# Performance work log

Measured on AMD Instinct MI355X. Metric: run time of the kernel, lower is better.

The kernel has to match this reference:

```python
import jax, jax.numpy as jnp
import numpy as np

B, L, D = 2, 8192, 1024


def setup_inputs() -> dict:
    key = jax.random.key(0)
    ks = jax.random.split(key, 6)
    x = jax.random.normal(ks[0], (B, L, D), dtype=jnp.float32)
    # phazor param init (torch): exp(2j*pi*arange(D)/D) * |randn(D)|
    mag = jnp.abs(jax.random.normal(ks[1], (D,), dtype=jnp.float32))
    ang = (2.0 * np.pi * jnp.arange(D) / D).astype(jnp.float32)
    phazor_real = mag * jnp.cos(ang)
    phazor_imag = mag * jnp.sin(ang)
    # phazor_init ~ complex randn
    phazor_init_real = jax.random.normal(ks[2], (D,), dtype=jnp.float32)
    phazor_init_imag = jax.random.normal(ks[3], (D,), dtype=jnp.float32)
    # last_conv_init ~ complex randn (first-call hidden state, broadcast over batch)
    last_conv_real = jax.random.normal(ks[4], (D,), dtype=jnp.float32)
    last_conv_imag = jax.random.normal(ks[5], (D,), dtype=jnp.float32)
    return {
        "x": x,
        "phazor_real": phazor_real, "phazor_imag": phazor_imag,
        "phazor_init_real": phazor_init_real, "phazor_init_imag": phazor_init_imag,
        "last_conv_real": last_conv_real, "last_conv_imag": last_conv_imag,
    }


def reference(x, phazor_real, phazor_imag, phazor_init_real, phazor_init_imag,
              last_conv_real, last_conv_imag):
    b, length, dim = x.shape
    dtype = x.dtype
    # reparameterized decay: magnitude exp(-|p|^2), keep angle of p
    ph = jnp.exp(-(phazor_real * phazor_real + phazor_imag * phazor_imag)) \
         * jnp.exp(1j * jnp.arctan2(phazor_imag, phazor_real))          # [D] complex
    # phazor_progression[t, d] = ph[d] ** t
    prog = jnp.power(ph[None, :], jnp.arange(length)[:, None])           # [L, D]
    pinit = phazor_init_real + 1j * phazor_init_imag                     # [D]
    filt = prog * pinit[None, :]                                         # [L, D]
    # FFT convolution with zero-padding to 2L (linear convolution)
    filt_fft = jnp.fft.fft(filt, n=2 * length, axis=0)                   # [2L, D]
    x_fft = jnp.fft.fft(x.astype(jnp.complex64), n=2 * length, axis=1)   # [B, 2L, D]
    conv = jnp.fft.ifft(filt_fft[None, :, :] * x_fft, axis=1)[:, :length, :]  # [B, L, D]
    # carry in hidden state from previous chunk (here: learned init, broadcast over batch)
    last = (last_conv_real + 1j * last_conv_imag)[None, None, :]          # [1, 1, D]
    conv_with_past = conv + last * prog[None, :, :] * ph[None, None, :]
    return conv_with_past.real.astype(dtype)
```

## Files before the change

### kernel.cpp

```cpp
#include <hip/hip_runtime.h>

#define BB 2
#define LL 8192
#define DD 1024
#define NC 128
#define TT 64

__device__ __forceinline__ void compute_ph(float pr, float pi, float& phr, float& phi) {
    float r2 = fmaf(pr, pr, pi * pi);
    float mag = expf(-r2);
    float r = sqrtf(r2);
    if (r > 1e-30f) {
        float inv = mag / r;
        phr = pr * inv;
        phi = pi * inv;
    } else {
        phr = mag;
        phi = 0.0f;
    }
}

__global__ __launch_bounds__(256) void k_partial(
    const float* __restrict__ x,
    const float* __restrict__ pr, const float* __restrict__ pi,
    const float* __restrict__ qr, const float* __restrict__ qi,
    float2* __restrict__ partial)
{
    int d = blockIdx.x * 256 + threadIdx.x;
    int j = blockIdx.y;
    int b = blockIdx.z;
    float phr, phi; compute_ph(pr[d], pi[d], phr, phi);
    float qre = qr[d], qim = qi[d];
    const float* xp = x + ((size_t)b * LL + (size_t)j * TT) * DD + d;
    float sr = 0.f, si = 0.f;
    #pragma unroll 16
    for (int t = 0; t < TT; ++t) {
        float xv = xp[(size_t)t * DD];
        float nr = fmaf(phr, sr, fmaf(-phi, si, qre * xv));
        float ni = fmaf(phi, sr, fmaf(phr, si, qim * xv));
        sr = nr; si = ni;
    }
    partial[((size_t)b * NC + j) * DD + d] = make_float2(sr, si);
}

__global__ __launch_bounds__(256) void k_final(
    const float* __restrict__ x,
    const float* __restrict__ pr, const float* __restrict__ pi,
    const float* __restrict__ qr, const float* __restrict__ qi,
    const float* __restrict__ lr, const float* __restrict__ li,
    const float2* __restrict__ partial,
    float* __restrict__ out)
{
    int d = blockIdx.x * 256 + threadIdx.x;
    int j = blockIdx.y;
    int b = blockIdx.z;
    float phr, phi; compute_ph(pr[d], pi[d], phr, phi);
    float qre = qr[d], qim = qi[d];

    float ar = phr, ai = phi;
    #pragma unroll
    for (int k = 0; k < 6; ++k) {
        float nr = ar * ar - ai * ai;
        float ni = 2.f * ar * ai;
        ar = nr; ai = ni;
    }

    float Sr = lr[d], Si = li[d];
    const float2* pb = partial + (size_t)b * NC * DD + d;
    #pragma unroll 4
    for (int k = 0; k < j; ++k) {
        float2 P = pb[(size_t)k * DD];
        float nr = fmaf(ar, Sr, fmaf(-ai, Si, P.x));
        float ni = fmaf(ai, Sr, fmaf(ar, Si, P.y));
        Sr = nr; Si = ni;
    }

    const size_t base = ((size_t)b * LL + (size_t)j * TT) * DD + d;
    const float* xp = x + base;
    float* op = out + base;
    #pragma unroll 16
    for (int t = 0; t < TT; ++t) {
        float xv = xp[(size_t)t * DD];
        float nr = fmaf(phr, Sr, fmaf(-phi, Si, qre * xv));
        float ni = fmaf(phi, Sr, fmaf(phr, Si, qim * xv));
        Sr = nr; Si = ni;
        op[(size_t)t * DD] = nr;
    }
}

extern "C" void kernel_launch(void* const* d_in, const int* in_sizes, int n_in,
                              void* d_out, int out_size, void* d_ws, size_t ws_size,
                              hipStream_t stream) {
    const float* x  = (const float*)d_in[0];
    const float* pr = (const float*)d_in[1];
    const float* pi = (const float*)d_in[2];
    const float* qr = (const float*)d_in[3];
    const float* qi = (const float*)d_in[4];
    const float* lr = (const float*)d_in[5];
    const float* li = (const float*)d_in[6];
    float* out = (float*)d_out;

    float2* partial = (float2*)d_ws;

    dim3 grid(DD / 256, NC, BB);
    k_partial<<<grid, 256, 0, stream>>>(x, pr, pi, qr, qi, partial);
    k_final<<<grid, 256, 0, stream>>>(x, pr, pi, qr, qi, lr, li, partial, out);
}
```

Baseline: 46.07 us.

## Split chunk-prefix carry into dedicated sequential scan kernel with prefetching

After: 51.68 us. 1.12x slower.

```diff
diff --git a/kernel.cpp b/kernel.cpp
--- a/kernel.cpp
+++ b/kernel.cpp
@@ -43,20 +43,18 @@
     partial[((size_t)b * NC + j) * DD + d] = make_float2(sr, si);
 }
 
-__global__ __launch_bounds__(256) void k_final(
-    const float* __restrict__ x,
+#define SCAN_DEPTH 16
+__global__ __launch_bounds__(256) void k_scan(
     const float* __restrict__ pr, const float* __restrict__ pi,
-    const float* __restrict__ qr, const float* __restrict__ qi,
     const float* __restrict__ lr, const float* __restrict__ li,
     const float2* __restrict__ partial,
-    float* __restrict__ out)
+    float2* __restrict__ Sarr)
 {
-    int d = blockIdx.x * 256 + threadIdx.x;
-    int j = blockIdx.y;
-    int b = blockIdx.z;
+    int idx = blockIdx.x * 256 + threadIdx.x;
+    int d = idx & (DD - 1);
+    int b = idx >> 10;
+
     float phr, phi; compute_ph(pr[d], pi[d], phr, phi);
-    float qre = qr[d], qim = qi[d];
-
     float ar = phr, ai = phi;
     #pragma unroll
     for (int k = 0; k < 6; ++k) {
@@ -67,13 +65,50 @@
 
     float Sr = lr[d], Si = li[d];
     const float2* pb = partial + (size_t)b * NC * DD + d;
-    #pragma unroll 4
-    for (int k = 0; k < j; ++k) {
-        float2 P = pb[(size_t)k * DD];
-        float nr = fmaf(ar, Sr, fmaf(-ai, Si, P.x));
-        float ni = fmaf(ai, Sr, fmaf(ar, Si, P.y));
-        Sr = nr; Si = ni;
+    float2* sb = Sarr + (size_t)b * NC * DD + d;
+
+    float2 buf[SCAN_DEPTH];
+    #pragma unroll
+    for (int u = 0; u < SCAN_DEPTH; ++u) buf[u] = pb[(size_t)u * DD];
+
+    #pragma unroll
+    for (int r = 0; r < NC / SCAN_DEPTH; ++r) {
+        float2 nxt[SCAN_DEPTH];
+        if (r < NC / SCAN_DEPTH - 1) {
+            #pragma unroll
+            for (int u = 0; u < SCAN_DEPTH; ++u)
+                nxt[u] = pb[(size_t)((r + 1) * SCAN_DEPTH + u) * DD];
+        }
+        #pragma unroll
+        for (int u = 0; u < SCAN_DEPTH; ++u) {
+            int j = r * SCAN_DEPTH + u;
+            sb[(size_t)j * DD] = make_float2(Sr, Si);
+            float nr = fmaf(ar, Sr, fmaf(-ai, Si, buf[u].x));
+            float ni = fmaf(ai, Sr, fmaf(ar, Si, buf[u].y));
+            Sr = nr; Si = ni;
+        }
+        if (r < NC / SCAN_DEPTH - 1) {
+            #pragma unroll
+            for (int u = 0; u < SCAN_DEPTH; ++u) buf[u] = nxt[u];
+        }
     }
+}
+
+__global__ __launch_bounds__(256) void k_final(
+    const float* __restrict__ x,
+    const float* __restrict__ pr, const float* __restrict__ pi,
+    const float* __restrict__ qr, const float* __restrict__ qi,
+    const float2* __restrict__ Sarr,
+    float* __restrict__ out)
+{
+    int d = blockIdx.x * 256 + threadIdx.x;
+    int j = blockIdx.y;
+    int b = blockIdx.z;
+    float phr, phi; compute_ph(pr[d], pi[d], phr, phi);
+    float qre = qr[d], qim = qi[d];
+
+    float2 S = Sarr[((size_t)b * NC + j) * DD + d];
+    float Sr = S.x, Si = S.y;
 
     const size_t base = ((size_t)b * LL + (size_t)j * TT) * DD + d;
     const float* xp = x + base;
@@ -84,7 +119,7 @@
         float nr = fmaf(phr, Sr, fmaf(-phi, Si, qre * xv));
         float ni = fmaf(phi, Sr, fmaf(phr, Si, qim * xv));
         Sr = nr; Si = ni;
-        op[(size_t)t * DD] = nr;
+        __builtin_nontemporal_store(nr, &op[(size_t)t * DD]);
     }
 }
 
@@ -101,8 +136,10 @@
     float* out = (float*)d_out;
 
     float2* partial = (float2*)d_ws;
+    float2* Sarr    = partial + (size_t)BB * NC * DD;
 
     dim3 grid(DD / 256, NC, BB);
     k_partial<<<grid, 256, 0, stream>>>(x, pr, pi, qr, qi, partial);
-    k_final<<<grid, 256, 0, stream>>>(x, pr, pi, qr, qi, lr, li, partial, out);
+    k_scan<<<(BB * DD) / 256, 256, 0, stream>>>(pr, pi, lr, li, partial, Sarr);
+    k_final<<<grid, 256, 0, stream>>>(x, pr, pi, qr, qi, Sarr, out);
 }
```

## Fuse partial and final scan kernels with a grid barrier, caching x in registers

Applied to the files above, without the earlier changes.

New measurement: 107.0 us. 2.32x slower.

```diff
diff --git a/kernel.cpp b/kernel.cpp
--- a/kernel.cpp
+++ b/kernel.cpp
@@ -3,8 +3,9 @@
 #define BB 2
 #define LL 8192
 #define DD 1024
-#define NC 128
-#define TT 64
+#define NC 64
+#define TT 128
+#define NBLK ((DD / 256) * NC * BB)
 
 __device__ __forceinline__ void compute_ph(float pr, float pi, float& phr, float& phi) {
     float r2 = fmaf(pr, pr, pi * pi);
@@ -20,46 +21,54 @@
     }
 }
 
-__global__ __launch_bounds__(256) void k_partial(
-    const float* __restrict__ x,
-    const float* __restrict__ pr, const float* __restrict__ pi,
-    const float* __restrict__ qr, const float* __restrict__ qi,
-    float2* __restrict__ partial)
-{
-    int d = blockIdx.x * 256 + threadIdx.x;
-    int j = blockIdx.y;
-    int b = blockIdx.z;
-    float phr, phi; compute_ph(pr[d], pi[d], phr, phi);
-    float qre = qr[d], qim = qi[d];
-    const float* xp = x + ((size_t)b * LL + (size_t)j * TT) * DD + d;
-    float sr = 0.f, si = 0.f;
-    #pragma unroll 16
-    for (int t = 0; t < TT; ++t) {
-        float xv = xp[(size_t)t * DD];
-        float nr = fmaf(phr, sr, fmaf(-phi, si, qre * xv));
-        float ni = fmaf(phi, sr, fmaf(phr, si, qim * xv));
-        sr = nr; si = ni;
-    }
-    partial[((size_t)b * NC + j) * DD + d] = make_float2(sr, si);
-}
-
-__global__ __launch_bounds__(256) void k_final(
+__global__ __launch_bounds__(256, 2) void k_fused(
     const float* __restrict__ x,
     const float* __restrict__ pr, const float* __restrict__ pi,
     const float* __restrict__ qr, const float* __restrict__ qi,
     const float* __restrict__ lr, const float* __restrict__ li,
-    const float2* __restrict__ partial,
+    float2* __restrict__ partial,
+    unsigned int* __restrict__ bar,
     float* __restrict__ out)
 {
-    int d = blockIdx.x * 256 + threadIdx.x;
-    int j = blockIdx.y;
-    int b = blockIdx.z;
+    const int d = blockIdx.x * 256 + threadIdx.x;
+    const int j = blockIdx.y;
+    const int b = blockIdx.z;
+
     float phr, phi; compute_ph(pr[d], pi[d], phr, phi);
-    float qre = qr[d], qim = qi[d];
+    const float qre = qr[d], qim = qi[d];
+
+    const size_t base = ((size_t)b * LL + (size_t)j * TT) * DD + d;
+    const float* xp = x + base;
+
+    float xv[TT];
+    #pragma unroll
+    for (int t = 0; t < TT; ++t) xv[t] = xp[(size_t)t * DD];
+
+    {
+        float sr = 0.f, si = 0.f;
+        #pragma unroll
+        for (int t = 0; t < TT; ++t) {
+            float nr = fmaf(phr, sr, fmaf(-phi, si, qre * xv[t]));
+            float ni = fmaf(phi, sr, fmaf(phr, si, qim * xv[t]));
+            sr = nr; si = ni;
+        }
+        partial[((size_t)b * NC + j) * DD + d] = make_float2(sr, si);
+    }
+
+    __syncthreads();
+    if (threadIdx.x == 0) {
+        __threadfence();
+        __hip_atomic_fetch_add(bar, 1u, __ATOMIC_ACQ_REL, __HIP_MEMORY_SCOPE_AGENT);
+        while (__hip_atomic_load(bar, __ATOMIC_ACQUIRE, __HIP_MEMORY_SCOPE_AGENT) < NBLK) {
+            __builtin_amdgcn_s_sleep(4);
+        }
+        __threadfence();
+    }
+    __syncthreads();
 
     float ar = phr, ai = phi;
     #pragma unroll
-    for (int k = 0; k < 6; ++k) {
+    for (int k = 0; k < 7; ++k) {
         float nr = ar * ar - ai * ai;
         float ni = 2.f * ar * ai;
         ar = nr; ai = ni;
@@ -75,14 +84,11 @@
         Sr = nr; Si = ni;
     }
 
-    const size_t base = ((size_t)b * LL + (size_t)j * TT) * DD + d;
-    const float* xp = x + base;
     float* op = out + base;
-    #pragma unroll 16
+    #pragma unroll
     for (int t = 0; t < TT; ++t) {
-        float xv = xp[(size_t)t * DD];
-        float nr = fmaf(phr, Sr, fmaf(-phi, Si, qre * xv));
-        float ni = fmaf(phi, Sr, fmaf(phr, Si, qim * xv));
+        float nr = fmaf(phr, Sr, fmaf(-phi, Si, qre * xv[t]));
+        float ni = fmaf(phi, Sr, fmaf(phr, Si, qim * xv[t]));
         Sr = nr; Si = ni;
         op[(size_t)t * DD] = nr;
     }
@@ -100,9 +106,11 @@
     const float* li = (const float*)d_in[6];
     float* out = (float*)d_out;
 
-    float2* partial = (float2*)d_ws;
+    unsigned int* bar = (unsigned int*)d_ws;
+    float2* partial = (float2*)((char*)d_ws + 1024);
+
+    hipMemsetAsync(d_ws, 0, 64, stream);
 
     dim3 grid(DD / 256, NC, BB);
-    k_partial<<<grid, 256, 0, stream>>>(x, pr, pi, qr, qi, partial);
-    k_final<<<grid, 256, 0, stream>>>(x, pr, pi, qr, qi, lr, li, partial, out);
+    k_fused<<<grid, 256, 0, stream>>>(x, pr, pi, qr, qi, lr, li, partial, bar, out);
 }
```

## Write local scan output in pass one and add decayed carry in pass two

Applied to the files above, without the earlier changes.

New measurement: 54.23 us. 17.7% more time.

```diff
diff --git a/kernel.cpp b/kernel.cpp
--- a/kernel.cpp
+++ b/kernel.cpp
@@ -5,6 +5,7 @@
 #define DD 1024
 #define NC 128
 #define TT 64
+#define NPAIR (DD/2)
 
 __device__ __forceinline__ void compute_ph(float pr, float pi, float& phr, float& phi) {
     float r2 = fmaf(pr, pr, pi * pi);
@@ -20,71 +21,102 @@
     }
 }
 
-__global__ __launch_bounds__(256) void k_partial(
+__global__ __launch_bounds__(256) void k_pass1(
     const float* __restrict__ x,
     const float* __restrict__ pr, const float* __restrict__ pi,
     const float* __restrict__ qr, const float* __restrict__ qi,
-    float2* __restrict__ partial)
+    float4* __restrict__ partial,
+    float* __restrict__ out)
 {
-    int d = blockIdx.x * 256 + threadIdx.x;
-    int j = blockIdx.y;
-    int b = blockIdx.z;
-    float phr, phi; compute_ph(pr[d], pi[d], phr, phi);
-    float qre = qr[d], qim = qi[d];
-    const float* xp = x + ((size_t)b * LL + (size_t)j * TT) * DD + d;
-    float sr = 0.f, si = 0.f;
+    const int p = blockIdx.x * 256 + threadIdx.x;
+    const int j = blockIdx.y;
+    const int b = blockIdx.z;
+    const int d0 = 2 * p, d1 = d0 + 1;
+
+    float phr0, phi0, phr1, phi1;
+    compute_ph(pr[d0], pi[d0], phr0, phi0);
+    compute_ph(pr[d1], pi[d1], phr1, phi1);
+    const float q0r = qr[d0], q0i = qi[d0], q1r = qr[d1], q1i = qi[d1];
+
+    const size_t rowbase = (size_t)b * LL + (size_t)j * TT;
+    const float2* xp = (const float2*)(x + rowbase * DD) + p;
+    float2* op = (float2*)(out + rowbase * DD) + p;
+
+    float sr0 = 0.f, si0 = 0.f, sr1 = 0.f, si1 = 0.f;
     #pragma unroll 16
     for (int t = 0; t < TT; ++t) {
-        float xv = xp[(size_t)t * DD];
-        float nr = fmaf(phr, sr, fmaf(-phi, si, qre * xv));
-        float ni = fmaf(phi, sr, fmaf(phr, si, qim * xv));
-        sr = nr; si = ni;
+        float2 xv = xp[(size_t)t * NPAIR];
+        float nr0 = fmaf(phr0, sr0, fmaf(-phi0, si0, q0r * xv.x));
+        float ni0 = fmaf(phi0, sr0, fmaf(phr0, si0, q0i * xv.x));
+        float nr1 = fmaf(phr1, sr1, fmaf(-phi1, si1, q1r * xv.y));
+        float ni1 = fmaf(phi1, sr1, fmaf(phr1, si1, q1i * xv.y));
+        sr0 = nr0; si0 = ni0; sr1 = nr1; si1 = ni1;
+        op[(size_t)t * NPAIR] = make_float2(nr0, nr1);
     }
-    partial[((size_t)b * NC + j) * DD + d] = make_float2(sr, si);
+    partial[((size_t)b * NC + j) * NPAIR + p] = make_float4(sr0, si0, sr1, si1);
 }
 
-__global__ __launch_bounds__(256) void k_final(
-    const float* __restrict__ x,
+__global__ __launch_bounds__(256) void k_pass2(
     const float* __restrict__ pr, const float* __restrict__ pi,
-    const float* __restrict__ qr, const float* __restrict__ qi,
     const float* __restrict__ lr, const float* __restrict__ li,
-    const float2* __restrict__ partial,
+    const float4* __restrict__ partial,
     float* __restrict__ out)
 {
-    int d = blockIdx.x * 256 + threadIdx.x;
-    int j = blockIdx.y;
-    int b = blockIdx.z;
-    float phr, phi; compute_ph(pr[d], pi[d], phr, phi);
-    float qre = qr[d], qim = qi[d];
+    const int p = blockIdx.x * 256 + threadIdx.x;
+    const int j = blockIdx.y;
+    const int b = blockIdx.z;
+    const int d0 = 2 * p, d1 = d0 + 1;
 
-    float ar = phr, ai = phi;
+    float phr0, phi0, phr1, phi1;
+    compute_ph(pr[d0], pi[d0], phr0, phi0);
+    compute_ph(pr[d1], pi[d1], phr1, phi1);
+
+    float a0r = phr0, a0i = phi0, a1r = phr1, a1i = phi1;
     #pragma unroll
     for (int k = 0; k < 6; ++k) {
-        float nr = ar * ar - ai * ai;
-        float ni = 2.f * ar * ai;
-        ar = nr; ai = ni;
+        float n0r = a0r * a0r - a0i * a0i, n0i = 2.f * a0r * a0i;
+        float n1r = a1r * a1r - a1i * a1i, n1i = 2.f * a1r * a1i;
+        a0r = n0r; a0i = n0i; a1r = n1r; a1i = n1i;
     }
 
-    float Sr = lr[d], Si = li[d];
-    const float2* pb = partial + (size_t)b * NC * DD + d;
-    #pragma unroll 4
-    for (int k = 0; k < j; ++k) {
-        float2 P = pb[(size_t)k * DD];
-        float nr = fmaf(ar, Sr, fmaf(-ai, Si, P.x));
-        float ni = fmaf(ai, Sr, fmaf(ar, Si, P.y));
-        Sr = nr; Si = ni;
+    float S0r = lr[d0], S0i = li[d0], S1r = lr[d1], S1i = li[d1];
+    const float4* pb = partial + (size_t)b * NC * NPAIR + p;
+    for (int bs = 0; bs < j; bs += 16) {
+        float4 buf[16];
+        #pragma unroll
+        for (int u = 0; u < 16; ++u) {
+            int k = bs + u;
+            int kc = (k < j) ? k : (j - 1);
+            buf[u] = pb[(size_t)kc * NPAIR];
+        }
+        #pragma unroll
+        for (int u = 0; u < 16; ++u) {
+            int k = bs + u;
+            if (k < j) {
+                float n0r = fmaf(a0r, S0r, fmaf(-a0i, S0i, buf[u].x));
+                float n0i = fmaf(a0i, S0r, fmaf(a0r, S0i, buf[u].y));
+                float n1r = fmaf(a1r, S1r, fmaf(-a1i, S1i, buf[u].z));
+                float n1i = fmaf(a1i, S1r, fmaf(a1r, S1i, buf[u].w));
+                S0r = n0r; S0i = n0i; S1r = n1r; S1i = n1i;
+            }
+        }
     }
 
-    const size_t base = ((size_t)b * LL + (size_t)j * TT) * DD + d;
-    const float* xp = x + base;
-    float* op = out + base;
+    float w0r = S0r * phr0 - S0i * phi0, w0i = S0r * phi0 + S0i * phr0;
+    float w1r = S1r * phr1 - S1i * phi1, w1i = S1r * phi1 + S1i * phr1;
+
+    const size_t rowbase = (size_t)b * LL + (size_t)j * TT;
+    float2* op = (float2*)(out + rowbase * DD) + p;
     #pragma unroll 16
     for (int t = 0; t < TT; ++t) {
-        float xv = xp[(size_t)t * DD];
-        float nr = fmaf(phr, Sr, fmaf(-phi, Si, qre * xv));
-        float ni = fmaf(phi, Sr, fmaf(phr, Si, qim * xv));
-        Sr = nr; Si = ni;
-        op[(size_t)t * DD] = nr;
+        float2 o = op[(size_t)t * NPAIR];
+        o.x += w0r; o.y += w1r;
+        op[(size_t)t * NPAIR] = o;
+        float n0r = fmaf(w0r, phr0, -(w0i * phi0));
+        float n0i = fmaf(w0r, phi0,  (w0i * phr0));
+        float n1r = fmaf(w1r, phr1, -(w1i * phi1));
+        float n1i = fmaf(w1r, phi1,  (w1i * phr1));
+        w0r = n0r; w0i = n0i; w1r = n1r; w1i = n1i;
     }
 }
 
@@ -100,9 +132,9 @@
     const float* li = (const float*)d_in[6];
     float* out = (float*)d_out;
 
-    float2* partial = (float2*)d_ws;
+    float4* partial = (float4*)d_ws;
 
-    dim3 grid(DD / 256, NC, BB);
-    k_partial<<<grid, 256, 0, stream>>>(x, pr, pi, qr, qi, partial);
-    k_final<<<grid, 256, 0, stream>>>(x, pr, pi, qr, qi, lr, li, partial, out);
+    dim3 grid(NPAIR / 256, NC, BB);
+    k_pass1<<<grid, 256, 0, stream>>>(x, pr, pi, qr, qi, partial, out);
+    k_pass2<<<grid, 256, 0, stream>>>(pr, pi, lr, li, partial, out);
 }
```
